# Optimization experiments

Hardware: AMD Instinct MI355X
Metric: run time of the kernel (lower is better)

Reference implementation:

```python
import jax, jax.numpy as jnp
import numpy as np

G, NP, C, H, L = 64, 512, 128, 4, 4
N = G * NP            # 32768 nodes
E = N * 16            # 524288 edges
HD = C // H
BN_EPS = 1e-5


def _bn(x, g, b):
    # BatchNorm1d, training-mode (biased batch statistics over nodes)
    m = x.mean(axis=0)
    v = jnp.var(x, axis=0)
    return (x - m) * jax.lax.rsqrt(v + BN_EPS) * g + b


def setup_inputs() -> dict:
    key = jax.random.key(0)
    ks = iter(jax.random.split(key, 64))
    rn = lambda shape, s=0.05: jax.random.normal(next(ks), shape, jnp.float32) * s
    inp = {}
    inp["x"] = jax.random.normal(next(ks), (N, 32), jnp.float32)
    inp["edge_attr"] = jax.random.normal(next(ks), (E, 16), jnp.float32)
    epg = E // G  # edges per graph; endpoints stay within each graph
    off = jnp.repeat(jnp.arange(G), epg) * NP
    src = jax.random.randint(next(ks), (E,), 0, NP) + off
    dst = jax.random.randint(next(ks), (E,), 0, NP) + off
    inp["edge_index"] = jnp.stack([src, dst]).astype(jnp.int32)
    inp["batch"] = jnp.repeat(jnp.arange(G), NP).astype(jnp.int32)
    inp["np_w"] = rn((32, C)); inp["np_b"] = jnp.zeros((C,), jnp.float32)
    inp["ep_w"] = rn((16, C)); inp["ep_b"] = jnp.zeros((C,), jnp.float32)
    inp["eps"] = jnp.zeros((L,), jnp.float32)  # GINEConv train_eps, init 0
    inp["gine_w1"] = rn((L, C, 2 * C)); inp["gine_b1"] = jnp.zeros((L, 2 * C), jnp.float32)
    inp["gine_w2"] = rn((L, 2 * C, C)); inp["gine_b2"] = jnp.zeros((L, C), jnp.float32)
    inp["attn_in_w"] = rn((L, 3 * C, C)); inp["attn_in_b"] = jnp.zeros((L, 3 * C), jnp.float32)
    inp["attn_out_w"] = rn((L, C, C)); inp["attn_out_b"] = jnp.zeros((L, C), jnp.float32)
    ones = jnp.ones((L, C), jnp.float32); zeros = jnp.zeros((L, C), jnp.float32)
    inp["bn1_g"], inp["bn1_b"] = ones, zeros
    inp["bn2_g"], inp["bn2_b"] = ones, zeros
    inp["bn3_g"], inp["bn3_b"] = ones, zeros
    inp["mlp_w1"] = rn((L, C, 2 * C)); inp["mlp_b1"] = jnp.zeros((L, 2 * C), jnp.float32)
    inp["mlp_w2"] = rn((L, 2 * C, C)); inp["mlp_b2"] = jnp.zeros((L, C), jnp.float32)
    inp["ln_g"] = jnp.ones((2 * C,), jnp.float32); inp["ln_b"] = jnp.zeros((2 * C,), jnp.float32)
    inp["head_w1"] = rn((2 * C, C)); inp["head_b1"] = jnp.zeros((C,), jnp.float32)
    inp["head_w2"] = rn((C, 1)); inp["head_b2"] = jnp.zeros((1,), jnp.float32)
    return inp


def reference(x, edge_attr, np_w, np_b, ep_w, ep_b, eps,
              gine_w1, gine_b1, gine_w2, gine_b2,
              attn_in_w, attn_in_b, attn_out_w, attn_out_b,
              bn1_g, bn1_b, bn2_g, bn2_b, bn3_g, bn3_b,
              mlp_w1, mlp_b1, mlp_w2, mlp_b2,
              ln_g, ln_b, head_w1, head_b1, head_w2, head_b2,
              edge_index, batch):
    h = x @ np_w + np_b                       # [N, C]
    e = edge_attr @ ep_w + ep_b               # [E, C]
    src, dst = edge_index[0], edge_index[1]   # PyG: row=source j, col=target i
    scale = 1.0 / np.sqrt(HD).astype(np.float32)
    for l in range(L):
        # ---- local GINEConv: relu(x_j + e) scatter-sum -> GELU MLP ----
        msg = jax.nn.relu(h[src] + e)                                 # [E, C]
        aggr = jax.ops.segment_sum(msg, dst, num_segments=N)          # [N, C]
        z = (1.0 + eps[l]) * h + aggr
        z = jax.nn.gelu(z @ gine_w1[l] + gine_b1[l], approximate=False) @ gine_w2[l] + gine_b2[l]
        h_local = _bn(z + h, bn1_g[l], bn1_b[l])
        # ---- global multihead attention on dense per-graph batch ----
        xd = h.reshape(G, NP, C)
        qkv = xd @ attn_in_w[l].T + attn_in_b[l]                      # [G, NP, 3C]
        q, k, v = jnp.split(qkv, 3, axis=-1)
        split_heads = lambda t: t.reshape(G, NP, H, HD).transpose(0, 2, 1, 3)
        q, k, v = split_heads(q), split_heads(k), split_heads(v)
        att = jax.nn.softmax(jnp.einsum('ghqd,ghkd->ghqk', q, k) * scale, axis=-1)
        o = jnp.einsum('ghqk,ghkd->ghqd', att, v).transpose(0, 2, 1, 3).reshape(N, C)
        o = o @ attn_out_w[l].T + attn_out_b[l]
        h_attn = _bn(o + h, bn2_g[l], bn2_b[l])
        # ---- combine + FFN ----
        out = h_local + h_attn
        m = jax.nn.relu(out @ mlp_w1[l] + mlp_b1[l]) @ mlp_w2[l] + mlp_b2[l]
        h = _bn(out + m, bn3_g[l], bn3_b[l])
    # ---- mean || max pooling over graphs ----
    cnt = jax.ops.segment_sum(jnp.ones((N, 1), h.dtype), batch, num_segments=G)
    x_mean = jax.ops.segment_sum(h, batch, num_segments=G) / cnt
    x_max = jax.ops.segment_max(h, batch, num_segments=G)
    g = jnp.concatenate([x_mean, x_max], axis=-1)                     # [G, 2C]
    mu = g.mean(-1, keepdims=True)
    var = jnp.var(g, axis=-1, keepdims=True)
    g = (g - mu) * jax.lax.rsqrt(var + 1e-5) * ln_g + ln_b
    g = jax.nn.gelu(g @ head_w1 + head_b1, approximate=False) @ head_w2 + head_b2
    return g.squeeze(-1)                                              # [G]
```

## Files before the change

kernel.cpp:

```cpp
#include <hip/hip_runtime.h>
#include <math.h>

typedef _Float16 f16;
typedef _Float16 f16x2 __attribute__((ext_vector_type(2)));
typedef _Float16 f16x4 __attribute__((ext_vector_type(4)));
typedef _Float16 f16x8 __attribute__((ext_vector_type(8)));
typedef float f32x4 __attribute__((ext_vector_type(4)));

#define G_ 64
#define NP_ 512
#define N_ 32768
#define E_ 524288
#define C_ 128
#define H_ 4
#define HD_ 32
#define L_ 4

static __device__ __forceinline__ float gelu_exact(float x) {
    return 0.5f * x * (1.0f + erff(x * 0.70710678118654752f));
}

__global__ __launch_bounds__(256) void k_prep(
    const float* __restrict__ g1, const float* __restrict__ g2,
    const float* __restrict__ m1, const float* __restrict__ m2,
    const float* __restrict__ ai, const float* __restrict__ ao,
    f16* __restrict__ g1t, f16* __restrict__ g2t,
    f16* __restrict__ m1t, f16* __restrict__ m2t,
    f16* __restrict__ ait, f16* __restrict__ aot)
{
    int i = blockIdx.x * 256 + threadIdx.x;
    if (i < 131072) {
        int l = i >> 15, r = i & 32767;
        int k = r >> 8, m = r & 255;
        g1t[l * 32768 + m * 128 + k] = (f16)g1[i];
    } else if (i < 262144) {
        int j = i - 131072;
        int l = j >> 15, r = j & 32767;
        int k = r >> 7, m = r & 127;
        g2t[l * 32768 + m * 256 + k] = (f16)g2[j];
    } else if (i < 393216) {
        int j = i - 262144;
        int l = j >> 15, r = j & 32767;
        int k = r >> 8, m = r & 255;
        m1t[l * 32768 + m * 128 + k] = (f16)m1[j];
    } else if (i < 524288) {
        int j = i - 393216;
        int l = j >> 15, r = j & 32767;
        int k = r >> 7, m = r & 127;
        m2t[l * 32768 + m * 256 + k] = (f16)m2[j];
    } else if (i < 720896) {
        int j = i - 524288;
        ait[j] = (f16)ai[j];
    } else if (i < 786432) {
        int j = i - 720896;
        aot[j] = (f16)ao[j];
    }
}

__global__ __launch_bounds__(256) void k_h0(const float* __restrict__ x,
    const float* __restrict__ w, const float* __restrict__ b,
    f16* __restrict__ h16)
{
    const int tid = threadIdx.x;
    const int lane = tid & 63, wid = tid >> 6;
    const int node = blockIdx.x * 4 + wid;
    const int c2 = lane * 2;
    float a0 = b[c2], a1 = b[c2 + 1];
    const float* xr = x + (size_t)node * 32;
#pragma unroll
    for (int k = 0; k < 32; k++) {
        float xv = xr[k];
        a0 += xv * w[k * 128 + c2];
        a1 += xv * w[k * 128 + c2 + 1];
    }
    f16x2 z; z[0] = (f16)a0; z[1] = (f16)a1;
    *(f16x2*)(h16 + (size_t)node * 128 + c2) = z;
}

__global__ void k_zero2(int* a, int* b) {
    int i = blockIdx.x * 256 + threadIdx.x;
    a[i] = 0; b[i] = 0;
}
__global__ void k_count(const int* __restrict__ ei, int* __restrict__ counts) {
    int e = blockIdx.x * 256 + threadIdx.x;
    atomicAdd(&counts[ei[E_ + e]], 1);
}
__global__ __launch_bounds__(1024) void k_scan(const int* __restrict__ counts,
                                               int* __restrict__ rowp)
{
    __shared__ int part[1024];
    const int t = threadIdx.x;
    int s = 0;
#pragma unroll
    for (int i = 0; i < 32; i++) s += counts[t * 32 + i];
    part[t] = s;
    __syncthreads();
    for (int off = 1; off < 1024; off <<= 1) {
        int u = (t >= off) ? part[t - off] : 0;
        __syncthreads();
        part[t] += u;
        __syncthreads();
    }
    int run = part[t] - s;
    for (int i = 0; i < 32; i++) {
        int c = counts[t * 32 + i];
        rowp[t * 32 + i] = run;
        run += c;
    }
    if (t == 1023) rowp[N_] = part[1023];
}
__global__ void k_fill(const int* __restrict__ ei, const int* __restrict__ rowp,
                       int* __restrict__ cursor, int* __restrict__ srcp,
                       int* __restrict__ eidp)
{
    int e = blockIdx.x * 256 + threadIdx.x;
    int d = ei[E_ + e];
    int p = atomicAdd(&cursor[d], 1);
    int pos = rowp[d] + p;
    srcp[pos] = ei[e];
    eidp[pos] = e;
}

__global__ __launch_bounds__(256) void k_edge(const float* __restrict__ edge_attr,
    const float* __restrict__ epw, const float* __restrict__ epb,
    const int* __restrict__ eidp, f16* __restrict__ e16p)
{
    __shared__ __align__(16) float rows[4][64][16];
    const int tid = threadIdx.x;
    const int lane = tid & 63, wid = tid >> 6;
    const int c2 = lane * 2;
    float w0[16], w1[16];
#pragma unroll
    for (int k = 0; k < 16; k++) {
        w0[k] = epw[k * 128 + c2];
        w1[k] = epw[k * 128 + c2 + 1];
    }
    const float b0 = epb[c2], b1 = epb[c2 + 1];
    const int base = blockIdx.x * 256 + wid * 64;
    const int eidv = eidp[base + lane];
    const int er = lane >> 2, ec = lane & 3;
#pragma unroll
    for (int u = 0; u < 4; u++) {
        int e = __shfl(eidv, u * 16 + er);
        float4 v = *(const float4*)(edge_attr + (size_t)e * 16 + ec * 4);
        *(float4*)(&rows[wid][u * 16 + er][ec * 4]) = v;
    }
    for (int i = 0; i < 64; i++) {
        const float* r = &rows[wid][i][0];
        float4 q0 = *(const float4*)(r);
        float4 q1 = *(const float4*)(r + 4);
        float4 q2 = *(const float4*)(r + 8);
        float4 q3 = *(const float4*)(r + 12);
        float e0 = b0, e1 = b1;
        e0 += q0.x*w0[0] + q0.y*w0[1] + q0.z*w0[2] + q0.w*w0[3]
            + q1.x*w0[4] + q1.y*w0[5] + q1.z*w0[6] + q1.w*w0[7]
            + q2.x*w0[8] + q2.y*w0[9] + q2.z*w0[10] + q2.w*w0[11]
            + q3.x*w0[12] + q3.y*w0[13] + q3.z*w0[14] + q3.w*w0[15];
        e1 += q0.x*w1[0] + q0.y*w1[1] + q0.z*w1[2] + q0.w*w1[3]
            + q1.x*w1[4] + q1.y*w1[5] + q1.z*w1[6] + q1.w*w1[7]
            + q2.x*w1[8] + q2.y*w1[9] + q2.z*w1[10] + q2.w*w1[11]
            + q3.x*w1[12] + q3.y*w1[13] + q3.z*w1[14] + q3.w*w1[15];
        f16x2 z; z[0] = (f16)e0; z[1] = (f16)e1;
        *(f16x2*)(e16p + (size_t)(base + i) * 128 + c2) = z;
    }
}

__global__ __launch_bounds__(256) void k_aggr(const f16* __restrict__ h16,
    const f16* __restrict__ e16p, const int* __restrict__ srcp,
    const int* __restrict__ rowp, const float* __restrict__ eps, int layer,
    f16* __restrict__ zin)
{
    const int tid = threadIdx.x;
    const int lane = tid & 63, wid = tid >> 6;
    const int node = blockIdx.x * 4 + wid;
    const int c2 = lane * 2;
    const int r0 = rowp[node], r1 = rowp[node + 1];
    const int deg = r1 - r0;
    const f16x2 hn = *(const f16x2*)(h16 + (size_t)node * 128 + c2);
    float a0 = 0.f, a1 = 0.f;
    if (deg > 0) {
        const int dd = deg < 64 ? deg : 64;
        const int jm = dd - 1;
        const int srcv = srcp[r0 + (lane < jm ? lane : jm)];
        f16x2 h_c, e_c, h_n, e_n;
        {
            int s = __shfl(srcv, 0);
            h_c = *(const f16x2*)(h16 + (size_t)s * 128 + c2);
            e_c = *(const f16x2*)(e16p + (size_t)r0 * 128 + c2);
            int j1 = 1 < jm ? 1 : jm;
            int s1 = __shfl(srcv, j1);
            h_n = *(const f16x2*)(h16 + (size_t)s1 * 128 + c2);
            e_n = *(const f16x2*)(e16p + (size_t)(r0 + j1) * 128 + c2);
        }
        for (int j = 0; j < dd; ++j) {
            int j2 = j + 2 < jm ? j + 2 : jm;
            int s2 = __shfl(srcv, j2);
            f16x2 h_f = *(const f16x2*)(h16 + (size_t)s2 * 128 + c2);
            f16x2 e_f = *(const f16x2*)(e16p + (size_t)(r0 + j2) * 128 + c2);
            a0 += fmaxf((float)e_c[0] + (float)h_c[0], 0.0f);
            a1 += fmaxf((float)e_c[1] + (float)h_c[1], 0.0f);
            h_c = h_n; e_c = e_n; h_n = h_f; e_n = e_f;
        }
        for (int pos = r0 + 64; pos < r1; ++pos) {
            int s = srcp[pos];
            f16x2 ev = *(const f16x2*)(e16p + (size_t)pos * 128 + c2);
            f16x2 hv = *(const f16x2*)(h16 + (size_t)s * 128 + c2);
            a0 += fmaxf((float)ev[0] + (float)hv[0], 0.0f);
            a1 += fmaxf((float)ev[1] + (float)hv[1], 0.0f);
        }
    }
    const float ep = 1.0f + eps[layer];
    f16x2 z;
    z[0] = (f16)(ep * (float)hn[0] + a0);
    z[1] = (f16)(ep * (float)hn[1] + a1);
    *(f16x2*)(zin + (size_t)node * 128 + c2) = z;
}

template <int KD, int EPI, bool COMB>
__global__ __launch_bounds__(256) void k_gemm(
    const f16* __restrict__ A, const f16* __restrict__ Bt,
    const float* __restrict__ bias,
    const f16* __restrict__ r1, const f16* __restrict__ r2,
    const float* __restrict__ sc1, const float* __restrict__ sc2,
    f16* __restrict__ out, f16* __restrict__ aout,
    float* __restrict__ stats, int Mout)
{
    __shared__ __align__(16) f16 As[64 * 40];
    __shared__ __align__(16) f16 Bs[128 * 40];
    __shared__ float sca[4][128];
    __shared__ float sscr[4][2][64];
    const int tid = threadIdx.x;
    const int lane = tid & 63, wid = tid >> 6;
    const int quad = lane >> 4, l16 = lane & 15;
    const int wm = wid >> 1, wn = wid & 1;
    const int rb = blockIdx.x, cb = blockIdx.y;
    if constexpr (COMB) {
        if (tid < 128) { sca[0][tid] = sc1[tid]; sca[1][tid] = sc1[128 + tid]; }
        else { int c = tid - 128; sca[2][c] = sc2[c]; sca[3][c] = sc2[128 + c]; }
    }
    f32x4 acc[2][4];
#pragma unroll
    for (int i = 0; i < 2; i++)
#pragma unroll
        for (int j = 0; j < 4; j++) acc[i][j] = {0.f, 0.f, 0.f, 0.f};
    const int arow0 = rb * 64, brow0 = cb * 128;
    const int srow = tid >> 2, sc4 = tid & 3;
#pragma unroll
    for (int kc = 0; kc < KD / 32; ++kc) {
        __syncthreads();
        if constexpr (COMB) {
            size_t off = (size_t)(arow0 + srow) * KD + kc * 32 + sc4 * 8;
            f16x8 x1 = *(const f16x8*)(r1 + off);
            f16x8 x2 = *(const f16x8*)(r2 + off);
            const int k0 = kc * 32 + sc4 * 8;
            f16x8 zc;
#pragma unroll
            for (int i = 0; i < 8; i++) {
                int k = k0 + i;
                float v = (float)x1[i] * sca[0][k] + sca[1][k]
                        + (float)x2[i] * sca[2][k] + sca[3][k];
                zc[i] = (f16)v;
            }
            *(f16x8*)(As + srow * 40 + sc4 * 8) = zc;
            if (cb == 0) *(f16x8*)(aout + off) = zc;
        } else {
            *(uint4*)(As + srow * 40 + sc4 * 8) =
                *(const uint4*)(A + (size_t)(arow0 + srow) * KD + kc * 32 + sc4 * 8);
        }
#pragma unroll
        for (int i = 0; i < 2; i++) {
            int j = tid + i * 256;
            int br = j >> 2, bc = j & 3;
            *(uint4*)(Bs + br * 40 + bc * 8) =
                *(const uint4*)(Bt + (size_t)(brow0 + br) * KD + kc * 32 + bc * 8);
        }
        __syncthreads();
        f16x8 af[2], bf[4];
#pragma unroll
        for (int mt = 0; mt < 2; mt++)
            af[mt] = *(const f16x8*)(As + (wm * 32 + mt * 16 + l16) * 40 + quad * 8);
#pragma unroll
        for (int nt = 0; nt < 4; nt++)
            bf[nt] = *(const f16x8*)(Bs + (wn * 64 + nt * 16 + l16) * 40 + quad * 8);
#pragma unroll
        for (int mt = 0; mt < 2; mt++)
#pragma unroll
            for (int nt = 0; nt < 4; nt++)
                acc[mt][nt] = __builtin_amdgcn_mfma_f32_16x16x32_f16(
                    af[mt], bf[nt], acc[mt][nt], 0, 0, 0);
    }
    float ssum[4] = {0, 0, 0, 0}, ssq[4] = {0, 0, 0, 0};
#pragma unroll
    for (int nt = 0; nt < 4; nt++) {
        const int col = cb * 128 + wn * 64 + nt * 16 + l16;
        const float bv = bias[col];
#pragma unroll
        for (int mt = 0; mt < 2; mt++) {
#pragma unroll
            for (int r = 0; r < 4; r++) {
                const int row = rb * 64 + wm * 32 + mt * 16 + quad * 4 + r;
                float v = acc[mt][nt][r] + bv;
                if constexpr (EPI == 0) v = gelu_exact(v);
                if constexpr (EPI == 1) v = fmaxf(v, 0.0f);
                if constexpr (EPI == 2) {
                    v += (float)r1[(size_t)row * 128 + col];
                    ssum[nt] += v;
                    ssq[nt] += v * v;
                }
                out[(size_t)row * Mout + col] = (f16)v;
            }
        }
    }
    if constexpr (EPI == 2) {
#pragma unroll
        for (int nt = 0; nt < 4; nt++) {
            float s = ssum[nt], q = ssq[nt];
            s += __shfl_xor(s, 16); s += __shfl_xor(s, 32);
            q += __shfl_xor(q, 16); q += __shfl_xor(q, 32);
            if (lane < 16) {
                sscr[wid][0][nt * 16 + lane] = s;
                sscr[wid][1][nt * 16 + lane] = q;
            }
        }
        __syncthreads();
        if (tid < 128) {
            int c = tid, wnc = c >> 6, jj = c & 63;
            stats[(size_t)rb * 256 + c] = sscr[wnc][0][jj] + sscr[wnc + 2][0][jj];
            stats[(size_t)rb * 256 + 128 + c] = sscr[wnc][1][jj] + sscr[wnc + 2][1][jj];
        }
    }
}

__global__ __launch_bounds__(256) void k_qkv(
    const f16* __restrict__ A, const f16* __restrict__ Bt,
    const float* __restrict__ bias,
    f16* __restrict__ qb, f16* __restrict__ kb, f16* __restrict__ vt)
{
    __shared__ __align__(16) f16 As[64 * 40];
    __shared__ __align__(16) f16 Bs[128 * 40];
    const int tid = threadIdx.x;
    const int lane = tid & 63, wid = tid >> 6;
    const int quad = lane >> 4, l16 = lane & 15;
    const int wm = wid >> 1, wn = wid & 1;
    const int rb = blockIdx.x, cb = blockIdx.y;
    f32x4 acc[2][4];
#pragma unroll
    for (int i = 0; i < 2; i++)
#pragma unroll
        for (int j = 0; j < 4; j++) acc[i][j] = {0.f, 0.f, 0.f, 0.f};
    const int arow0 = rb * 64, brow0 = cb * 128;
    const int srow = tid >> 2, sc4 = tid & 3;
#pragma unroll
    for (int kc = 0; kc < 4; ++kc) {
        __syncthreads();
        *(uint4*)(As + srow * 40 + sc4 * 8) =
            *(const uint4*)(A + (size_t)(arow0 + srow) * 128 + kc * 32 + sc4 * 8);
#pragma unroll
        for (int i = 0; i < 2; i++) {
            int j = tid + i * 256;
            int br = j >> 2, bc = j & 3;
            *(uint4*)(Bs + br * 40 + bc * 8) =
                *(const uint4*)(Bt + (size_t)(brow0 + br) * 128 + kc * 32 + bc * 8);
        }
        __syncthreads();
        f16x8 af[2], bf[4];
#pragma unroll
        for (int mt = 0; mt < 2; mt++)
            af[mt] = *(const f16x8*)(As + (wm * 32 + mt * 16 + l16) * 40 + quad * 8);
#pragma unroll
        for (int nt = 0; nt < 4; nt++)
            bf[nt] = *(const f16x8*)(Bs + (wn * 64 + nt * 16 + l16) * 40 + quad * 8);
#pragma unroll
        for (int mt = 0; mt < 2; mt++)
#pragma unroll
            for (int nt = 0; nt < 4; nt++)
                acc[mt][nt] = __builtin_amdgcn_mfma_f32_16x16x32_f16(
                    af[mt], bf[nt], acc[mt][nt], 0, 0, 0);
    }
    if (cb < 2) {
        f16* outp = cb ? kb : qb;
#pragma unroll
        for (int nt = 0; nt < 4; nt++) {
            const int col = wn * 64 + nt * 16 + l16;
            const float bv = bias[cb * 128 + col];
#pragma unroll
            for (int mt = 0; mt < 2; mt++) {
#pragma unroll
                for (int r = 0; r < 4; r++) {
                    const int row = rb * 64 + wm * 32 + mt * 16 + quad * 4 + r;
                    outp[(size_t)row * 128 + col] = (f16)(acc[mt][nt][r] + bv);
                }
            }
        }
    } else {
        const int g = rb >> 3;
#pragma unroll
        for (int nt = 0; nt < 4; nt++) {
            const int coll = wn * 64 + nt * 16 + l16;
            const int h = coll >> 5, d = coll & 31;
            const float bv = bias[256 + coll];
#pragma unroll
            for (int mt = 0; mt < 2; mt++) {
                const int n0 = (rb & 7) * 64 + wm * 32 + mt * 16 + quad * 4;
                f16x4 z;
#pragma unroll
                for (int r = 0; r < 4; r++) z[r] = (f16)(acc[mt][nt][r] + bv);
                *(f16x4*)(vt + ((size_t)((g * 4 + h) * 32 + d)) * 512 + n0) = z;
            }
        }
    }
}

__global__ __launch_bounds__(1024) void k_fin(
    const float* __restrict__ sA, const float* __restrict__ sB,
    const float* __restrict__ g1, const float* __restrict__ b1,
    const float* __restrict__ g2, const float* __restrict__ b2,
    float* __restrict__ o1, float* __restrict__ o2)
{
    __shared__ float rS[8][128], rQ[8][128];
    const float* s = blockIdx.x ? sB : sA;
    const float* g = blockIdx.x ? g2 : g1;
    const float* bb = blockIdx.x ? b2 : b1;
    float* o = blockIdx.x ? o2 : o1;
    const int c = threadIdx.x & 127, seg = threadIdx.x >> 7;
    float S = 0, Q = 0;
    for (int b = seg * 64; b < seg * 64 + 64; b++) {
        S += s[b * 256 + c];
        Q += s[b * 256 + 128 + c];
    }
    rS[seg][c] = S; rQ[seg][c] = Q;
    __syncthreads();
    if (threadIdx.x < 128) {
        float Ss = 0, Qs = 0;
#pragma unroll
        for (int k = 0; k < 8; k++) { Ss += rS[k][c]; Qs += rQ[k][c]; }
        float mean = Ss * (1.0f / 32768.0f);
        float var = Qs * (1.0f / 32768.0f) - mean * mean;
        float rstd = rsqrtf(var + 1e-5f);
        float scv = g[c] * rstd;
        o[c] = scv;
        o[128 + c] = bb[c] - mean * scv;
    }
}

__global__ __launch_bounds__(256) void k_bn3(const f16* __restrict__ t3,
    const float* __restrict__ s3, f16* __restrict__ h16)
{
    int i = blockIdx.x * 256 + threadIdx.x;
    int n = i >> 6, c2 = (i & 63) * 2;
    f16x2 a = *(const f16x2*)(t3 + (size_t)n * 128 + c2);
    f16x2 z;
    z[0] = (f16)((float)a[0] * s3[c2] + s3[128 + c2]);
    z[1] = (f16)((float)a[1] * s3[c2 + 1] + s3[129 + c2]);
    *(f16x2*)(h16 + (size_t)n * 128 + c2) = z;
}

__global__ __launch_bounds__(256) void k_attn(const f16* __restrict__ qb,
    const f16* __restrict__ kb, const f16* __restrict__ vt, f16* __restrict__ o)
{
    __shared__ __align__(16) f16 Ks[512 * 32];
    __shared__ __align__(16) f16 Ps[4][16 * 56];
    const int tid = threadIdx.x;
    const int lane = tid & 63, wid = tid >> 6;
    const int quad = lane >> 4, l16 = lane & 15;
    const int blk = blockIdx.x;
    const int gh = blk >> 3, qc = blk & 7;
    const int g = gh >> 2, h = gh & 3;
#pragma unroll
    for (int i = 0; i < 8; i++) {
        int j = i * 256 + tid;
        int n = j >> 2, c4 = j & 3;
        *(uint4*)(Ks + n * 32 + c4 * 8) =
            *(const uint4*)(kb + (size_t)(g * 512 + n) * 128 + h * 32 + c4 * 8);
    }
    const int node = g * 512 + qc * 64 + wid * 16 + l16;
    f16x8 aq = *(const f16x8*)(qb + (size_t)node * 128 + h * 32 + quad * 8);
    __syncthreads();
    const f32x4 zero = {0.f, 0.f, 0.f, 0.f};
    const float cexp = 0.17677669529663689f * 1.44269504088896341f;
    float mx[4] = {-1e30f, -1e30f, -1e30f, -1e30f};
    for (int kt = 0; kt < 32; ++kt) {
        f16x8 bk = *(const f16x8*)(Ks + (kt * 16 + l16) * 32 + quad * 8);
        f32x4 s = __builtin_amdgcn_mfma_f32_16x16x32_f16(aq, bk, zero, 0, 0, 0);
#pragma unroll
        for (int r = 0; r < 4; r++) mx[r] = fmaxf(mx[r], s[r]);
    }
#pragma unroll
    for (int r = 0; r < 4; r++) {
        float m = mx[r];
        m = fmaxf(m, __shfl_xor(m, 1)); m = fmaxf(m, __shfl_xor(m, 2));
        m = fmaxf(m, __shfl_xor(m, 4)); m = fmaxf(m, __shfl_xor(m, 8));
        mx[r] = m;
    }
    float lsum[4] = {0, 0, 0, 0};
    f32x4 o0 = {0.f, 0.f, 0.f, 0.f}, o1 = {0.f, 0.f, 0.f, 0.f};
    f16* pp = &Ps[wid][0];
    const f16* vbase = vt + (size_t)gh * 32 * 512;
    for (int ch = 0; ch < 16; ++ch) {
#pragma unroll
        for (int hf = 0; hf < 2; ++hf) {
            int kt = ch * 2 + hf;
            f16x8 bk = *(const f16x8*)(Ks + (kt * 16 + l16) * 32 + quad * 8);
            f32x4 s = __builtin_amdgcn_mfma_f32_16x16x32_f16(aq, bk, zero, 0, 0, 0);
#pragma unroll
            for (int r = 0; r < 4; r++) {
                float p = exp2f((s[r] - mx[r]) * cexp);
                lsum[r] += p;
                pp[(quad * 4 + r) * 56 + hf * 16 + l16] = (f16)p;
            }
        }
        f16x8 ap = *(const f16x8*)(pp + l16 * 56 + quad * 8);
        f16x8 bv0 = *(const f16x8*)(vbase + (size_t)l16 * 512 + ch * 32 + quad * 8);
        f16x8 bv1 = *(const f16x8*)(vbase + (size_t)(16 + l16) * 512 + ch * 32 + quad * 8);
        o0 = __builtin_amdgcn_mfma_f32_16x16x32_f16(ap, bv0, o0, 0, 0, 0);
        o1 = __builtin_amdgcn_mfma_f32_16x16x32_f16(ap, bv1, o1, 0, 0, 0);
    }
#pragma unroll
    for (int r = 0; r < 4; r++) {
        float s = lsum[r];
        s += __shfl_xor(s, 1); s += __shfl_xor(s, 2);
        s += __shfl_xor(s, 4); s += __shfl_xor(s, 8);
        lsum[r] = 1.0f / s;
    }
#pragma unroll
    for (int r = 0; r < 4; r++) {
        int nrow = g * 512 + qc * 64 + wid * 16 + quad * 4 + r;
        o[(size_t)nrow * 128 + h * 32 + l16] = (f16)(o0[r] * lsum[r]);
        o[(size_t)nrow * 128 + h * 32 + 16 + l16] = (f16)(o1[r] * lsum[r]);
    }
}

__global__ __launch_bounds__(256) void k_pool(const f16* __restrict__ h16,
    const float* __restrict__ ln_g, const float* __restrict__ ln_b,
    const float* __restrict__ w1, const float* __restrict__ b1,
    const float* __restrict__ w2, const float* __restrict__ b2,
    float* __restrict__ outp)
{
    __shared__ float ssum[4][128], smax[4][128];
    __shared__ float gl[256];
    __shared__ float red[256];
    __shared__ float hid[128];
    __shared__ float stat[2];
    const int tid = threadIdx.x, lane = tid & 63, wid = tid >> 6;
    const int g = blockIdx.x;
    const int c2 = lane * 2;
    float s0 = 0, s1 = 0, m0 = -1e30f, m1 = -1e30f;
    for (int i = 0; i < 128; i++) {
        int n = g * 512 + i * 4 + wid;
        f16x2 hv = *(const f16x2*)(h16 + (size_t)n * 128 + c2);
        float v0 = (float)hv[0], v1 = (float)hv[1];
        s0 += v0; s1 += v1;
        m0 = fmaxf(m0, v0); m1 = fmaxf(m1, v1);
    }
    ssum[wid][c2] = s0; ssum[wid][c2 + 1] = s1;
    smax[wid][c2] = m0; smax[wid][c2 + 1] = m1;
    __syncthreads();
    if (tid < 128) {
        float S = ssum[0][tid] + ssum[1][tid] + ssum[2][tid] + ssum[3][tid];
        float M = fmaxf(fmaxf(smax[0][tid], smax[1][tid]),
                        fmaxf(smax[2][tid], smax[3][tid]));
        gl[tid] = S * (1.0f / 512.0f);
        gl[128 + tid] = M;
    }
    __syncthreads();
    float v = gl[tid];
    red[tid] = v;
    __syncthreads();
    for (int off = 128; off > 0; off >>= 1) {
        if (tid < off) red[tid] += red[tid + off];
        __syncthreads();
    }
    if (tid == 0) stat[0] = red[0] * (1.0f / 256.0f);
    __syncthreads();
    float mu = stat[0];
    red[tid] = (v - mu) * (v - mu);
    __syncthreads();
    for (int off = 128; off > 0; off >>= 1) {
        if (tid < off) red[tid] += red[tid + off];
        __syncthreads();
    }
    if (tid == 0) stat[1] = rsqrtf(red[0] * (1.0f / 256.0f) + 1e-5f);
    __syncthreads();
    float gn = (v - mu) * stat[1] * ln_g[tid] + ln_b[tid];
    __syncthreads();
    gl[tid] = gn;
    __syncthreads();
    if (tid < 128) {
        float a = b1[tid];
        for (int k = 0; k < 256; k++) a += gl[k] * w1[k * 128 + tid];
        hid[tid] = gelu_exact(a);
    }
    __syncthreads();
    if (tid < 64) {
        float a = hid[tid] * w2[tid] + hid[tid + 64] * w2[tid + 64];
        a += __shfl_xor(a, 32); a += __shfl_xor(a, 16); a += __shfl_xor(a, 8);
        a += __shfl_xor(a, 4); a += __shfl_xor(a, 2); a += __shfl_xor(a, 1);
        if (tid == 0) outp[g] = a + b2[0];
    }
}

extern "C" void kernel_launch(void* const* d_in, const int* in_sizes, int n_in,
                              void* d_out, int out_size, void* d_ws, size_t ws_size,
                              hipStream_t stream)
{
    const float* x          = (const float*)d_in[0];
    const float* edge_attr  = (const float*)d_in[1];
    const int*   ei         = (const int*)d_in[2];
    const float* np_w       = (const float*)d_in[4];
    const float* np_b       = (const float*)d_in[5];
    const float* ep_w       = (const float*)d_in[6];
    const float* ep_b       = (const float*)d_in[7];
    const float* eps        = (const float*)d_in[8];
    const float* gine_w1    = (const float*)d_in[9];
    const float* gine_b1    = (const float*)d_in[10];
    const float* gine_w2    = (const float*)d_in[11];
    const float* gine_b2    = (const float*)d_in[12];
    const float* attn_in_w  = (const float*)d_in[13];
    const float* attn_in_b  = (const float*)d_in[14];
    const float* attn_out_w = (const float*)d_in[15];
    const float* attn_out_b = (const float*)d_in[16];
    const float* bn1_g      = (const float*)d_in[17];
    const float* bn1_b      = (const float*)d_in[18];
    const float* bn2_g      = (const float*)d_in[19];
    const float* bn2_b      = (const float*)d_in[20];
    const float* bn3_g      = (const float*)d_in[21];
    const float* bn3_b      = (const float*)d_in[22];
    const float* mlp_w1     = (const float*)d_in[23];
    const float* mlp_b1     = (const float*)d_in[24];
    const float* mlp_w2     = (const float*)d_in[25];
    const float* mlp_b2     = (const float*)d_in[26];
    const float* ln_g       = (const float*)d_in[27];
    const float* ln_b       = (const float*)d_in[28];
    const float* head_w1    = (const float*)d_in[29];
    const float* head_b1    = (const float*)d_in[30];
    const float* head_w2    = (const float*)d_in[31];
    const float* head_b2    = (const float*)d_in[32];

    char* ws = (char*)d_ws;
    size_t off = 0;
    auto alloc = [&](size_t bytes) {
        void* p = ws + off;
        off += (bytes + 255) & ~(size_t)255;
        return p;
    };
    f16*  h16    = (f16*)alloc((size_t)N_ * 128 * 2);
    f16*  zin    = (f16*)alloc((size_t)N_ * 128 * 2);
    f16*  tloc   = (f16*)alloc((size_t)N_ * 128 * 2);
    f16*  tattn  = (f16*)alloc((size_t)N_ * 128 * 2);
    f16*  out16  = (f16*)alloc((size_t)N_ * 128 * 2);
    f16*  o16    = (f16*)alloc((size_t)N_ * 128 * 2);
    f16*  u16    = (f16*)alloc((size_t)N_ * 256 * 2);
    float* statsA = (float*)alloc(512 * 256 * 4);
    float* statsB = (float*)alloc(512 * 256 * 4);
    float* scsh1  = (float*)alloc(256 * 4);
    float* scsh2  = (float*)alloc(256 * 4);
    float* scsh3  = (float*)alloc(256 * 4);
    int*  rowp   = (int*)alloc((N_ + 1) * 4);
    int*  counts = (int*)alloc(N_ * 4);
    int*  cursor = (int*)alloc(N_ * 4);
    int*  srcp   = (int*)alloc((size_t)E_ * 4);
    int*  eidp   = (int*)alloc((size_t)E_ * 4);
    f16*  g1t    = (f16*)alloc((size_t)L_ * 32768 * 2);
    f16*  g2t    = (f16*)alloc((size_t)L_ * 32768 * 2);
    f16*  m1t    = (f16*)alloc((size_t)L_ * 32768 * 2);
    f16*  m2t    = (f16*)alloc((size_t)L_ * 32768 * 2);
    f16*  ait    = (f16*)alloc((size_t)L_ * 49152 * 2);
    f16*  aot    = (f16*)alloc((size_t)L_ * 16384 * 2);
    f16*  e16p   = (f16*)alloc((size_t)E_ * 128 * 2);
    f16*  qbuf = zin;
    f16*  kbuf = out16;
    f16*  vt   = u16 + (size_t)N_ * 128;

    dim3 B(256);
    k_prep<<<dim3(3072), B, 0, stream>>>(gine_w1, gine_w2, mlp_w1, mlp_w2,
                                         attn_in_w, attn_out_w,
                                         g1t, g2t, m1t, m2t, ait, aot);
    k_h0<<<dim3(8192), B, 0, stream>>>(x, np_w, np_b, h16);
    k_zero2<<<dim3(128), B, 0, stream>>>(counts, cursor);
    k_count<<<dim3(2048), B, 0, stream>>>(ei, counts);
    k_scan<<<dim3(1), dim3(1024), 0, stream>>>(counts, rowp);
    k_fill<<<dim3(2048), B, 0, stream>>>(ei, rowp, cursor, srcp, eidp);
    k_edge<<<dim3(2048), B, 0, stream>>>(edge_attr, ep_w, ep_b, eidp, e16p);

    const f16* nf = (const f16*)nullptr;
    const float* nff = (const float*)nullptr;
    for (int l = 0; l < L_; l++) {
        k_aggr<<<dim3(8192), B, 0, stream>>>(h16, e16p, srcp, rowp, eps, l, zin);
        k_gemm<128, 0, false><<<dim3(512, 2), B, 0, stream>>>(
            zin, g1t + l * 32768, gine_b1 + l * 256, nf, nf, nff, nff,
            u16, (f16*)nullptr, (float*)nullptr, 256);
        k_gemm<256, 2, false><<<dim3(512, 1), B, 0, stream>>>(
            u16, g2t + l * 32768, gine_b2 + l * 128, h16, nf, nff, nff,
            tloc, (f16*)nullptr, statsA, 128);
        k_qkv<<<dim3(512, 3), B, 0, stream>>>(
            h16, ait + l * 49152, attn_in_b + l * 384, qbuf, kbuf, vt);
        k_attn<<<dim3(2048), B, 0, stream>>>(qbuf, kbuf, vt, o16);
        k_gemm<128, 2, false><<<dim3(512, 1), B, 0, stream>>>(
            o16, aot + l * 16384, attn_out_b + l * 128, h16, nf, nff, nff,
            tattn, (f16*)nullptr, statsB, 128);
        k_fin<<<dim3(2), dim3(1024), 0, stream>>>(
            statsA, statsB, bn1_g + l * 128, bn1_b + l * 128,
            bn2_g + l * 128, bn2_b + l * 128, scsh1, scsh2);
        k_gemm<128, 1, true><<<dim3(512, 2), B, 0, stream>>>(
            nf, m1t + l * 32768, mlp_b1 + l * 256, tloc, tattn, scsh1, scsh2,
            u16, out16, (float*)nullptr, 256);
        k_gemm<256, 2, false><<<dim3(512, 1), B, 0, stream>>>(
            u16, m2t + l * 32768, mlp_b2 + l * 128, out16, nf, nff, nff,
            zin, (f16*)nullptr, statsA, 128);
        k_fin<<<dim3(1), dim3(1024), 0, stream>>>(
            statsA, statsA, bn3_g + l * 128, bn3_b + l * 128,
            bn3_g + l * 128, bn3_b + l * 128, scsh3, scsh3);
        k_bn3<<<dim3(8192), B, 0, stream>>>(zin, scsh3, h16);
    }
    k_pool<<<dim3(64), B, 0, stream>>>(h16, ln_g, ln_b, head_w1, head_b1,
                                       head_w2, head_b2, (float*)d_out);
}
```

Baseline: 960.9 us.

## Transpose attention score MFMA, pad LDS rows, and interleave block-to-graph mapping

Attention now computes S^T by swapping the MFMA operands. Each lane then holds scores for a single query row, so the row max and row sum need only two cross-lane shuffles instead of per-register four-step reductions. P is written to LDS as packed f16x4 stores, and K/P rows are padded to 40 halfs to reduce bank conflicts. Block indices in the edge, aggregation and attention kernels are remapped so consecutive blocks touch different graphs, changing cache/L2 locality and load spread. The locality change could help or hurt depending on L2 behaviour.

```diff
diff --git a/kernel.cpp b/kernel.cpp
--- a/kernel.cpp
+++ b/kernel.cpp
@@ -136,7 +136,8 @@
         w1[k] = epw[k * 128 + c2 + 1];
     }
     const float b0 = epb[c2], b1 = epb[c2 + 1];
-    const int base = blockIdx.x * 256 + wid * 64;
+    const int gidx = blockIdx.x & 63, chunk = blockIdx.x >> 6;
+    const int base = (gidx * 32 + chunk) * 256 + wid * 64;
     const int eidv = eidp[base + lane];
     const int er = lane >> 2, ec = lane & 3;
 #pragma unroll
@@ -172,7 +173,7 @@
 {
     const int tid = threadIdx.x;
     const int lane = tid & 63, wid = tid >> 6;
-    const int node = blockIdx.x * 4 + wid;
+    const int node = (blockIdx.x & 63) * 512 + (blockIdx.x >> 6) * 4 + wid;
     const int c2 = lane * 2;
     const int r0 = rowp[node], r1 = rowp[node + 1];
     const int deg = r1 - r0;
@@ -458,19 +459,19 @@
 __global__ __launch_bounds__(256) void k_attn(const f16* __restrict__ qb,
     const f16* __restrict__ kb, const f16* __restrict__ vt, f16* __restrict__ o)
 {
-    __shared__ __align__(16) f16 Ks[512 * 32];
-    __shared__ __align__(16) f16 Ps[4][16 * 56];
+    __shared__ __align__(16) f16 Ks[512 * 40];
+    __shared__ __align__(16) f16 Ps[4][16 * 40];
     const int tid = threadIdx.x;
     const int lane = tid & 63, wid = tid >> 6;
     const int quad = lane >> 4, l16 = lane & 15;
     const int blk = blockIdx.x;
-    const int gh = blk >> 3, qc = blk & 7;
+    const int gh = blk & 255, qc = blk >> 8;
     const int g = gh >> 2, h = gh & 3;
 #pragma unroll
     for (int i = 0; i < 8; i++) {
         int j = i * 256 + tid;
         int n = j >> 2, c4 = j & 3;
-        *(uint4*)(Ks + n * 32 + c4 * 8) =
+        *(uint4*)(Ks + n * 40 + c4 * 8) =
             *(const uint4*)(kb + (size_t)(g * 512 + n) * 128 + h * 32 + c4 * 8);
     }
     const int node = g * 512 + qc * 64 + wid * 16 + l16;
@@ -478,21 +479,15 @@
     __syncthreads();
     const f32x4 zero = {0.f, 0.f, 0.f, 0.f};
     const float cexp = 0.17677669529663689f * 1.44269504088896341f;
-    float mx[4] = {-1e30f, -1e30f, -1e30f, -1e30f};
+    float mx = -1e30f;
     for (int kt = 0; kt < 32; ++kt) {
-        f16x8 bk = *(const f16x8*)(Ks + (kt * 16 + l16) * 32 + quad * 8);
-        f32x4 s = __builtin_amdgcn_mfma_f32_16x16x32_f16(aq, bk, zero, 0, 0, 0);
-#pragma unroll
-        for (int r = 0; r < 4; r++) mx[r] = fmaxf(mx[r], s[r]);
-    }
-#pragma unroll
-    for (int r = 0; r < 4; r++) {
-        float m = mx[r];
-        m = fmaxf(m, __shfl_xor(m, 1)); m = fmaxf(m, __shfl_xor(m, 2));
-        m = fmaxf(m, __shfl_xor(m, 4)); m = fmaxf(m, __shfl_xor(m, 8));
-        mx[r] = m;
-    }
-    float lsum[4] = {0, 0, 0, 0};
+        f16x8 ak = *(const f16x8*)(Ks + (kt * 16 + l16) * 40 + quad * 8);
+        f32x4 s = __builtin_amdgcn_mfma_f32_16x16x32_f16(ak, aq, zero, 0, 0, 0);
+        mx = fmaxf(mx, fmaxf(fmaxf(s[0], s[1]), fmaxf(s[2], s[3])));
+    }
+    mx = fmaxf(mx, __shfl_xor(mx, 16));
+    mx = fmaxf(mx, __shfl_xor(mx, 32));
+    float lsum = 0.f;
     f32x4 o0 = {0.f, 0.f, 0.f, 0.f}, o1 = {0.f, 0.f, 0.f, 0.f};
     f16* pp = &Ps[wid][0];
     const f16* vbase = vt + (size_t)gh * 32 * 512;
@@ -500,33 +495,32 @@
 #pragma unroll
         for (int hf = 0; hf < 2; ++hf) {
             int kt = ch * 2 + hf;
-            f16x8 bk = *(const f16x8*)(Ks + (kt * 16 + l16) * 32 + quad * 8);
-            f32x4 s = __builtin_amdgcn_mfma_f32_16x16x32_f16(aq, bk, zero, 0, 0, 0);
+            f16x8 ak = *(const f16x8*)(Ks + (kt * 16 + l16) * 40 + quad * 8);
+            f32x4 s = __builtin_amdgcn_mfma_f32_16x16x32_f16(ak, aq, zero, 0, 0, 0);
+            f16x4 pk;
 #pragma unroll
             for (int r = 0; r < 4; r++) {
-                float p = exp2f((s[r] - mx[r]) * cexp);
-                lsum[r] += p;
-                pp[(quad * 4 + r) * 56 + hf * 16 + l16] = (f16)p;
+                float p = exp2f((s[r] - mx) * cexp);
+                lsum += p;
+                pk[r] = (f16)p;
             }
-        }
-        f16x8 ap = *(const f16x8*)(pp + l16 * 56 + quad * 8);
+            *(f16x4*)(pp + l16 * 40 + hf * 16 + quad * 4) = pk;
+        }
+        f16x8 ap = *(const f16x8*)(pp + l16 * 40 + quad * 8);
         f16x8 bv0 = *(const f16x8*)(vbase + (size_t)l16 * 512 + ch * 32 + quad * 8);
         f16x8 bv1 = *(const f16x8*)(vbase + (size_t)(16 + l16) * 512 + ch * 32 + quad * 8);
         o0 = __builtin_amdgcn_mfma_f32_16x16x32_f16(ap, bv0, o0, 0, 0, 0);
         o1 = __builtin_amdgcn_mfma_f32_16x16x32_f16(ap, bv1, o1, 0, 0, 0);
     }
+    lsum += __shfl_xor(lsum, 16);
+    lsum += __shfl_xor(lsum, 32);
+    const float linv = 1.0f / lsum;
 #pragma unroll
     for (int r = 0; r < 4; r++) {
-        float s = lsum[r];
-        s += __shfl_xor(s, 1); s += __shfl_xor(s, 2);
-        s += __shfl_xor(s, 4); s += __shfl_xor(s, 8);
-        lsum[r] = 1.0f / s;
-    }
-#pragma unroll
-    for (int r = 0; r < 4; r++) {
+        float li = __shfl(linv, quad * 4 + r);
         int nrow = g * 512 + qc * 64 + wid * 16 + quad * 4 + r;
-        o[(size_t)nrow * 128 + h * 32 + l16] = (f16)(o0[r] * lsum[r]);
-        o[(size_t)nrow * 128 + h * 32 + 16 + l16] = (f16)(o1[r] * lsum[r]);
+        o[(size_t)nrow * 128 + h * 32 + l16] = (f16)(o0[r] * li);
+        o[(size_t)nrow * 128 + h * 32 + 16 + l16] = (f16)(o1[r] * li);
     }
 }
 
```

Measured after the change: 1.003 ms. +4.3%, slower.
